# Kernel optimization log

Hardware: AMD Instinct MI355X
Metric: run time of the kernel (lower is better)

## Reference

```python
import jax, jax.numpy as jnp
import numpy as np

HEADS = 8
DIM_HEAD = 32
GROUPS = 8
EPS = 1e-5


def setup_inputs() -> dict:
    key = jax.random.key(0)
    k0, k1, k2 = jax.random.split(key, 3)
    dim = 256
    inner = HEADS * DIM_HEAD  # 256
    x = jax.random.normal(k0, (1, dim, 16, 16, 16), dtype=jnp.float32)
    gn_weight = jnp.ones((dim,), dtype=jnp.float32)
    gn_bias = jnp.zeros((dim,), dtype=jnp.float32)
    w_qkv = jax.random.normal(k1, (3 * inner, dim), dtype=jnp.float32) * 0.02
    w_out = jax.random.normal(k2, (dim, inner), dtype=jnp.float32) * 0.02
    b_out = jnp.zeros((dim,), dtype=jnp.float32)
    return {"x": x, "gn_weight": gn_weight, "gn_bias": gn_bias,
            "w_qkv": w_qkv, "w_out": w_out, "b_out": b_out}


def reference(x, gn_weight, gn_bias, w_qkv, w_out, b_out):
    b, c, d, h, w = x.shape
    n = d * h * w  # tokens

    # --- GroupNorm(8, c) with affine ---
    xg = x.reshape(b, GROUPS, c // GROUPS, n)
    mean = xg.mean(axis=(2, 3), keepdims=True)
    var = xg.var(axis=(2, 3), keepdims=True)
    xn = ((xg - mean) * jax.lax.rsqrt(var + EPS)).reshape(b, c, n)
    xn = xn * gn_weight[:, None] + gn_bias[:, None]

    # --- 1x1 Conv3d QKV projection (no bias) ---
    qkv = jnp.einsum('bcn,oc->bon', xn, w_qkv)              # (b, 3*H*dh, n)
    qkv = qkv.reshape(b, 3, HEADS, DIM_HEAD, n)
    q, k, v = qkv[:, 0], qkv[:, 1], qkv[:, 2]               # each (b, H, dh, n)

    # --- naive softmax attention over n = d*h*w tokens ---
    scale = DIM_HEAD ** (-0.5)
    sim = jnp.einsum('bhdi,bhdj->bhij', q, k) * scale       # (b, H, n, n)
    attn = jax.nn.softmax(sim, axis=-1)
    out = jnp.einsum('bhij,bhdj->bhdi', attn, v)            # (b, H, dh, n)
    out = out.reshape(b, HEADS * DIM_HEAD, n)

    # --- 1x1 Conv3d output projection (with bias) ---
    y = jnp.einsum('bcn,oc->bon', out, w_out) + b_out[:, None]
    return y.reshape(b, c, d, h, w)
```

## Files before the change

### kernel.cpp

```cpp
#include <hip/hip_runtime.h>
#include <hip/hip_bf16.h>
#include <math.h>


#define LOG2E 1.4426950408889634f

typedef __attribute__((ext_vector_type(8))) short bf16x8;
typedef __attribute__((ext_vector_type(4))) short bf16x4;
typedef __attribute__((ext_vector_type(4))) float f32x4;
typedef __attribute__((ext_vector_type(4))) unsigned short u16x4;

__device__ inline unsigned short f2bf(float f) {
  __hip_bfloat16 h = __float2bfloat16(f);
  return *reinterpret_cast<unsigned short*>(&h);
}

__device__ inline bf16x4 pack4_bf(float p0, float p1, float p2, float p3) {
  float2 a, b;
  a.x = p0; a.y = p1; b.x = p2; b.y = p3;
  __hip_bfloat162 lo = __float22bfloat162_rn(a);
  __hip_bfloat162 hi = __float22bfloat162_rn(b);
  union U { __hip_bfloat162 h2[2]; bf16x4 v; } u;
  u.h2[0] = lo; u.h2[1] = hi;
  return u.v;
}

__global__ __launch_bounds__(256) void xt_kernel(const float* __restrict__ x,
                                                 unsigned short* __restrict__ xTb) {
  __shared__ float tile[64][65];
  int nb = blockIdx.x * 64, cb = blockIdx.y * 64;
  int tn = threadIdx.x & 63, t4 = threadIdx.x >> 6;
#pragma unroll
  for (int i = 0; i < 16; ++i) {
    int cc = t4 + i * 4;
    tile[cc][tn] = x[(size_t)(cb + cc) * 4096 + nb + tn];
  }
  __syncthreads();
#pragma unroll
  for (int i = 0; i < 16; ++i) {
    int nn = t4 + i * 4;
    xTb[(size_t)(nb + nn) * 256 + cb + tn] = f2bf(tile[tn][nn]);
  }
}

__global__ __launch_bounds__(256) void gn_part_kernel(const float* __restrict__ x,
                                                      float* __restrict__ psum) {
  int bi = blockIdx.x;
  const float4* p = reinterpret_cast<const float4*>(x) + (size_t)bi * 512 + threadIdx.x;
  float4 v1 = p[0];
  float4 v2 = p[256];
  float s = (v1.x + v1.y) + (v1.z + v1.w) + (v2.x + v2.y) + (v2.z + v2.w);
  float q = (v1.x * v1.x + v1.y * v1.y) + (v1.z * v1.z + v1.w * v1.w) +
            (v2.x * v2.x + v2.y * v2.y) + (v2.z * v2.z + v2.w * v2.w);
  for (int off = 32; off > 0; off >>= 1) {
    s += __shfl_down(s, off);
    q += __shfl_down(q, off);
  }
  __shared__ float ss[4], sq[4];
  int w = threadIdx.x >> 6, lane = threadIdx.x & 63;
  if (lane == 0) { ss[w] = s; sq[w] = q; }
  __syncthreads();
  if (threadIdx.x == 0) {
    psum[bi * 2 + 0] = (ss[0] + ss[1]) + (ss[2] + ss[3]);
    psum[bi * 2 + 1] = (sq[0] + sq[1]) + (sq[2] + sq[3]);
  }
}

__global__ __launch_bounds__(64) void gn_final_kernel(const float* __restrict__ psum,
                                                      float* __restrict__ stats) {
  int g = blockIdx.x;
  int lane = threadIdx.x;
  float s = psum[(g * 64 + lane) * 2 + 0];
  float q = psum[(g * 64 + lane) * 2 + 1];
  for (int off = 32; off > 0; off >>= 1) {
    s += __shfl_down(s, off);
    q += __shfl_down(q, off);
  }
  if (lane == 0) {
    float mean = s * (1.f / 131072.f);
    float var = q * (1.f / 131072.f) - mean * mean;
    stats[g * 2 + 0] = mean;
    stats[g * 2 + 1] = rsqrtf(var + 1e-5f);
  }
}

__global__ __launch_bounds__(256) void fold_kernel(const float* __restrict__ w_qkv,
                                                   const float* __restrict__ gnw,
                                                   const float* __restrict__ gnb,
                                                   const float* __restrict__ stats,
                                                   unsigned short* __restrict__ w2b,
                                                   float* __restrict__ bias0) {
  int wid = (blockIdx.x * 256 + threadIdx.x) >> 6;
  int lane = threadIdx.x & 63;
  float part = 0.f;
#pragma unroll
  for (int cc = 0; cc < 4; ++cc) {
    int c = lane + cc * 64;
    int g = c >> 5;
    float mean = stats[2 * g], rstd = stats[2 * g + 1];
    float al = rstd * gnw[c];
    float be = gnb[c] - mean * al;
    float wv = w_qkv[wid * 256 + c];
    w2b[wid * 256 + c] = f2bf(wv * al);
    part += wv * be;
  }
  for (int off = 32; off > 0; off >>= 1) part += __shfl_down(part, off);
  if (lane == 0) bias0[wid] = part;
}

__global__ __launch_bounds__(256) void wout_cast_kernel(const float* __restrict__ w_out,
                                                        unsigned short* __restrict__ w_outb) {
  int i = (blockIdx.x * 256 + threadIdx.x) * 4;
  float4 v = *(const float4*)(w_out + i);
  u16x4 o;
  o[0] = f2bf(v.x); o[1] = f2bf(v.y); o[2] = f2bf(v.z); o[3] = f2bf(v.w);
  *(u16x4*)(w_outb + i) = o;
}

__global__ __launch_bounds__(256) void gemm_qkv_mfma(const unsigned short* __restrict__ w2b,
                                                     const unsigned short* __restrict__ xTb,
                                                     const float* __restrict__ bias0,
                                                     unsigned short* __restrict__ qt,
                                                     unsigned short* __restrict__ ktb,
                                                     unsigned short* __restrict__ v16) {
  const int nb = blockIdx.x, mb = blockIdx.y;
  const int t = threadIdx.x;
  const int w = t >> 6, lane = t & 63;
  const int c = lane & 15, g = lane >> 4;
  const int m0 = mb * 64 + w * 16;
  const int n0 = nb * 64;
  const f32x4 zero4 = {0.f, 0.f, 0.f, 0.f};

  const unsigned short* ap = w2b + (size_t)(m0 + c) * 256 + g * 8;
  bf16x8 af[8];
#pragma unroll
  for (int ks = 0; ks < 8; ++ks) af[ks] = *(const bf16x8*)(ap + ks * 32);

  f32x4 acc[4] = {zero4, zero4, zero4, zero4};
  const unsigned short* bp = xTb + (size_t)(n0 + c) * 256 + g * 8;
#pragma unroll
  for (int half = 0; half < 2; ++half) {
    bf16x8 bf[4][4];
#pragma unroll
    for (int nt = 0; nt < 4; ++nt)
#pragma unroll
      for (int k2 = 0; k2 < 4; ++k2)
        bf[nt][k2] = *(const bf16x8*)(bp + (size_t)nt * 4096 + half * 128 + k2 * 32);
#pragma unroll
    for (int k2 = 0; k2 < 4; ++k2)
#pragma unroll
      for (int nt = 0; nt < 4; ++nt)
        acc[nt] = __builtin_amdgcn_mfma_f32_16x16x32_bf16(af[half * 4 + k2], bf[nt][k2],
                                                          acc[nt], 0, 0, 0);
  }

  const int o0 = m0 + g * 4;
  const int t3 = o0 >> 8;
  const int h = (o0 >> 5) & 7;
  const int d0 = o0 & 31;
  float b4[4];
#pragma unroll
  for (int r = 0; r < 4; ++r) b4[r] = bias0[o0 + r];
#pragma unroll
  for (int nt = 0; nt < 4; ++nt) {
    int n = n0 + nt * 16 + c;
    if (t3 == 0) {
      u16x4 v;
#pragma unroll
      for (int r = 0; r < 4; ++r) v[r] = f2bf((acc[nt][r] + b4[r]) * 0.17677669529663687f);
      *(u16x4*)(qt + (size_t)(h * 4096 + n) * 32 + d0) = v;
    } else if (t3 == 1) {
      u16x4 v;
#pragma unroll
      for (int r = 0; r < 4; ++r) v[r] = f2bf(acc[nt][r] + b4[r]);
      *(u16x4*)(ktb + (size_t)(h * 4096 + n) * 32 + d0) = v;
    } else {
#pragma unroll
      for (int r = 0; r < 4; ++r)
        v16[(size_t)((h * 256 + (n >> 4)) * 32 + d0 + r) * 16 + (n & 15)] =
            f2bf(acc[nt][r] + b4[r]);
    }
  }
}

__global__ __launch_bounds__(256) void attn_mfma_kernel(const unsigned short* __restrict__ qt,
                                                        const unsigned short* __restrict__ ktb,
                                                        const unsigned short* __restrict__ v16,
                                                        unsigned short* __restrict__ outTb) {
  const int b = blockIdx.x;
  const int h = b & 7;
  const int i0 = (b >> 3) * 64;
  const int t = threadIdx.x;
  const int w = t >> 6;
  const int lane = t & 63;
  const int c = lane & 15;
  const int g = lane >> 4;
  const f32x4 zero4 = {0.f, 0.f, 0.f, 0.f};

  const unsigned short* qb = qt + (size_t)h * 131072 + (size_t)(i0 + c) * 32 + g * 8;
  bf16x8 qf[4];
#pragma unroll
  for (int it = 0; it < 4; ++it) qf[it] = *(const bf16x8*)(qb + it * 512);

  const unsigned short* kp = ktb + (size_t)h * 131072 + (size_t)(w * 1024 + c) * 32 + g * 8;
  const unsigned short* vp = v16 + (size_t)((h * 256 + w * 64) * 32 + c) * 16 + g * 4;

  float l[4] = {0.f, 0.f, 0.f, 0.f};
  f32x4 oacc[4][2];
#pragma unroll
  for (int it = 0; it < 4; ++it) {
    oacc[it][0] = zero4;
    oacc[it][1] = zero4;
  }

  bf16x8 kf[4], kn[4];
#pragma unroll
  for (int js = 0; js < 4; ++js) kf[js] = *(const bf16x8*)(kp + js * 512);

#pragma unroll 1
  for (int jt = 0; jt < 16; ++jt) {
    bf16x4 vf[2][4];
#pragma unroll
    for (int dh = 0; dh < 2; ++dh)
#pragma unroll
      for (int js = 0; js < 4; ++js)
        vf[dh][js] = *(const bf16x4*)(vp + (jt * 4 + js) * 512 + dh * 256);
    int jn = (jt < 15) ? jt + 1 : 15;
#pragma unroll
    for (int js = 0; js < 4; ++js)
      kn[js] = *(const bf16x8*)(kp + jn * 2048 + js * 512);

#pragma unroll
    for (int it = 0; it < 4; ++it) {
      f32x4 st[4];
#pragma unroll
      for (int js = 0; js < 4; ++js)
        st[js] = __builtin_amdgcn_mfma_f32_16x16x32_bf16(kf[js], qf[it], zero4, 0, 0, 0);
      bf16x4 pb[4];
      float lsum = 0.f;
#pragma unroll
      for (int js = 0; js < 4; ++js) {
        float p0 = __builtin_amdgcn_exp2f(st[js][0] * LOG2E);
        float p1 = __builtin_amdgcn_exp2f(st[js][1] * LOG2E);
        float p2 = __builtin_amdgcn_exp2f(st[js][2] * LOG2E);
        float p3 = __builtin_amdgcn_exp2f(st[js][3] * LOG2E);
        lsum += (p0 + p1) + (p2 + p3);
        pb[js] = pack4_bf(p0, p1, p2, p3);
      }
      l[it] += lsum;
#pragma unroll
      for (int js = 0; js < 4; ++js) {
        oacc[it][0] = __builtin_amdgcn_mfma_f32_16x16x16bf16_1k(vf[0][js], pb[js], oacc[it][0], 0, 0, 0);
        oacc[it][1] = __builtin_amdgcn_mfma_f32_16x16x16bf16_1k(vf[1][js], pb[js], oacc[it][1], 0, 0, 0);
      }
    }
#pragma unroll
    for (int js = 0; js < 4; ++js) kf[js] = kn[js];
  }

  __shared__ float lds_o[4][4][2][4][4][17];
  __shared__ float lds_l[4][4][16];
#pragma unroll
  for (int it = 0; it < 4; ++it) {
    float lv = l[it];
    lv += __shfl_xor(lv, 16);
    lv += __shfl_xor(lv, 32);
    if (g == 0) lds_l[w][it][c] = lv;
#pragma unroll
    for (int dh = 0; dh < 2; ++dh)
#pragma unroll
      for (int r = 0; r < 4; ++r)
        lds_o[w][it][dh][g][r][c] = oacc[it][dh][r];
  }
  __syncthreads();
  {
    const int it = w;
    float L = (lds_l[0][it][c] + lds_l[1][it][c]) + (lds_l[2][it][c] + lds_l[3][it][c]);
    float inv = 1.f / L;
#pragma unroll
    for (int dh = 0; dh < 2; ++dh) {
      u16x4 o;
#pragma unroll
      for (int r = 0; r < 4; ++r) {
        float v = ((lds_o[0][it][dh][g][r][c] + lds_o[1][it][dh][g][r][c]) +
                   (lds_o[2][it][dh][g][r][c] + lds_o[3][it][dh][g][r][c]));
        o[r] = f2bf(v * inv);
      }
      *(u16x4*)(outTb + (size_t)(i0 + it * 16 + c) * 256 + h * 32 + dh * 16 + g * 4) = o;
    }
  }
}

__global__ __launch_bounds__(256) void gemm_out_mfma(const unsigned short* __restrict__ w_outb,
                                                     const unsigned short* __restrict__ outTb,
                                                     const float* __restrict__ bias,
                                                     float* __restrict__ y) {
  const int nb = blockIdx.x, mb = blockIdx.y;
  const int t = threadIdx.x;
  const int w = t >> 6, lane = t & 63;
  const int c = lane & 15, g = lane >> 4;
  const int m0 = mb * 64 + w * 16;
  const int n0 = nb * 64;
  const f32x4 zero4 = {0.f, 0.f, 0.f, 0.f};

  const unsigned short* ap = w_outb + (size_t)(m0 + c) * 256 + g * 8;
  bf16x8 af[8];
#pragma unroll
  for (int ks = 0; ks < 8; ++ks) af[ks] = *(const bf16x8*)(ap + ks * 32);

  f32x4 acc[4] = {zero4, zero4, zero4, zero4};
  const unsigned short* bp = outTb + (size_t)(n0 + c) * 256 + g * 8;
#pragma unroll
  for (int half = 0; half < 2; ++half) {
    bf16x8 bf[4][4];
#pragma unroll
    for (int nt = 0; nt < 4; ++nt)
#pragma unroll
      for (int k2 = 0; k2 < 4; ++k2)
        bf[nt][k2] = *(const bf16x8*)(bp + (size_t)nt * 4096 + half * 128 + k2 * 32);
#pragma unroll
    for (int k2 = 0; k2 < 4; ++k2)
#pragma unroll
      for (int nt = 0; nt < 4; ++nt)
        acc[nt] = __builtin_amdgcn_mfma_f32_16x16x32_bf16(af[half * 4 + k2], bf[nt][k2],
                                                          acc[nt], 0, 0, 0);
  }

  const int o0 = m0 + g * 4;
  float b4[4];
#pragma unroll
  for (int r = 0; r < 4; ++r) b4[r] = bias[o0 + r];
#pragma unroll
  for (int nt = 0; nt < 4; ++nt) {
    int n = n0 + nt * 16 + c;
#pragma unroll
    for (int r = 0; r < 4; ++r)
      y[(size_t)(o0 + r) * 4096 + n] = acc[nt][r] + b4[r];
  }
}

extern "C" void kernel_launch(void* const* d_in, const int* in_sizes, int n_in,
                              void* d_out, int out_size, void* d_ws, size_t ws_size,
                              hipStream_t stream) {
  const float* x = (const float*)d_in[0];
  const float* gnw = (const float*)d_in[1];
  const float* gnb = (const float*)d_in[2];
  const float* w_qkv = (const float*)d_in[3];
  const float* w_out = (const float*)d_in[4];
  const float* b_out = (const float*)d_in[5];
  float* ws = (float*)d_ws;

  float* psum = ws;
  float* stats = ws + 1024;
  float* bias0 = ws + 1088;
  unsigned short* w2b = (unsigned short*)(ws + 2048);
  unsigned short* w_outb = w2b + 196608;
  unsigned short* xTb = w_outb + 65536;
  unsigned short* qt = xTb + 1048576;
  unsigned short* ktb = qt + 1048576;
  unsigned short* v16 = ktb + 1048576;
  unsigned short* outTb = v16 + 1048576;
  float* y = (float*)d_out;

  hipLaunchKernelGGL(xt_kernel, dim3(64, 4), dim3(256), 0, stream, x, xTb);
  hipLaunchKernelGGL(gn_part_kernel, dim3(512), dim3(256), 0, stream, x, psum);
  hipLaunchKernelGGL(gn_final_kernel, dim3(8), dim3(64), 0, stream, psum, stats);
  hipLaunchKernelGGL(fold_kernel, dim3(192), dim3(256), 0, stream, w_qkv, gnw, gnb, stats, w2b, bias0);
  hipLaunchKernelGGL(wout_cast_kernel, dim3(64), dim3(256), 0, stream, w_out, w_outb);
  hipLaunchKernelGGL(gemm_qkv_mfma, dim3(64, 12), dim3(256), 0, stream, w2b, xTb, bias0, qt, ktb, v16);
  hipLaunchKernelGGL(attn_mfma_kernel, dim3(512), dim3(256), 0, stream, qt, ktb, v16, outTb);
  hipLaunchKernelGGL(gemm_out_mfma, dim3(64, 4), dim3(256), 0, stream, w_outb, outTb, b_out, y);
}
```

Baseline: 74.62 us.

## Fuse GroupNorm stats into transpose, merge fold kernels, widen attention to 8 waves

Computes the GroupNorm partial sums inside the transpose kernel and merges the stats-finalize, weight-fold and w_out cast into one kernel, cutting the launch count from eight to five and avoiding a second read of x. Folds log2(e) into the Q scale so the softmax exp2 needs no multiply. The attention kernel now runs 512 threads, splitting the key range across 8 waves, and raises wave priority around the MFMA sections. The cost is a larger cross-wave LDS reduction and more register pressure per block.

```diff
diff --git a/kernel.cpp b/kernel.cpp
--- a/kernel.cpp
+++ b/kernel.cpp
@@ -2,8 +2,6 @@
 #include <hip/hip_bf16.h>
 #include <math.h>
 
-
-#define LOG2E 1.4426950408889634f
 
 typedef __attribute__((ext_vector_type(8))) short bf16x8;
 typedef __attribute__((ext_vector_type(4))) short bf16x4;
@@ -25,17 +23,39 @@
   return u.v;
 }
 
-__global__ __launch_bounds__(256) void xt_kernel(const float* __restrict__ x,
-                                                 unsigned short* __restrict__ xTb) {
+__global__ __launch_bounds__(256) void xt_gn_kernel(const float* __restrict__ x,
+                                                    unsigned short* __restrict__ xTb,
+                                                    float2* __restrict__ psum2) {
   __shared__ float tile[64][65];
+  __shared__ float red[4][4];
   int nb = blockIdx.x * 64, cb = blockIdx.y * 64;
   int tn = threadIdx.x & 63, t4 = threadIdx.x >> 6;
+  float slo = 0.f, qlo = 0.f, shi = 0.f, qhi = 0.f;
 #pragma unroll
   for (int i = 0; i < 16; ++i) {
     int cc = t4 + i * 4;
-    tile[cc][tn] = x[(size_t)(cb + cc) * 4096 + nb + tn];
+    float v = x[(size_t)(cb + cc) * 4096 + nb + tn];
+    tile[cc][tn] = v;
+    if (i < 8) { slo += v; qlo += v * v; } else { shi += v; qhi += v * v; }
+  }
+#pragma unroll
+  for (int off = 32; off > 0; off >>= 1) {
+    slo += __shfl_down(slo, off); qlo += __shfl_down(qlo, off);
+    shi += __shfl_down(shi, off); qhi += __shfl_down(qhi, off);
+  }
+  if ((threadIdx.x & 63) == 0) {
+    red[t4][0] = slo; red[t4][1] = qlo; red[t4][2] = shi; red[t4][3] = qhi;
   }
   __syncthreads();
+  if (threadIdx.x == 0) {
+    float a = (red[0][0] + red[1][0]) + (red[2][0] + red[3][0]);
+    float b = (red[0][1] + red[1][1]) + (red[2][1] + red[3][1]);
+    psum2[(blockIdx.y * 2) * 64 + blockIdx.x] = make_float2(a, b);
+  } else if (threadIdx.x == 64) {
+    float a = (red[0][2] + red[1][2]) + (red[2][2] + red[3][2]);
+    float b = (red[0][3] + red[1][3]) + (red[2][3] + red[3][3]);
+    psum2[(blockIdx.y * 2 + 1) * 64 + blockIdx.x] = make_float2(a, b);
+  }
 #pragma unroll
   for (int i = 0; i < 16; ++i) {
     int nn = t4 + i * 4;
@@ -43,78 +63,67 @@
   }
 }
 
-__global__ __launch_bounds__(256) void gn_part_kernel(const float* __restrict__ x,
-                                                      float* __restrict__ psum) {
-  int bi = blockIdx.x;
-  const float4* p = reinterpret_cast<const float4*>(x) + (size_t)bi * 512 + threadIdx.x;
-  float4 v1 = p[0];
-  float4 v2 = p[256];
-  float s = (v1.x + v1.y) + (v1.z + v1.w) + (v2.x + v2.y) + (v2.z + v2.w);
-  float q = (v1.x * v1.x + v1.y * v1.y) + (v1.z * v1.z + v1.w * v1.w) +
-            (v2.x * v2.x + v2.y * v2.y) + (v2.z * v2.z + v2.w * v2.w);
-  for (int off = 32; off > 0; off >>= 1) {
-    s += __shfl_down(s, off);
-    q += __shfl_down(q, off);
-  }
-  __shared__ float ss[4], sq[4];
-  int w = threadIdx.x >> 6, lane = threadIdx.x & 63;
-  if (lane == 0) { ss[w] = s; sq[w] = q; }
+__global__ __launch_bounds__(256) void fold_all_kernel(const float* __restrict__ w_qkv,
+                                                       const float* __restrict__ gnw,
+                                                       const float* __restrict__ gnb,
+                                                       const float2* __restrict__ psum2,
+                                                       const float* __restrict__ w_out,
+                                                       unsigned short* __restrict__ w2b,
+                                                       float* __restrict__ bias0,
+                                                       unsigned short* __restrict__ w_outb) {
+  int bid = blockIdx.x;
+  int t = threadIdx.x;
+  if (bid >= 192) {
+    int i = ((bid - 192) * 256 + t) * 4;
+    float4 v = *(const float4*)(w_out + i);
+    u16x4 o;
+    o[0] = f2bf(v.x); o[1] = f2bf(v.y); o[2] = f2bf(v.z); o[3] = f2bf(v.w);
+    *(u16x4*)(w_outb + i) = o;
+    return;
+  }
+  __shared__ float sm[8], sr[8];
+  __shared__ float s_al[256], s_be[256];
+  {
+    int g = t >> 5, ii = t & 31;
+    float2 p0 = psum2[g * 64 + ii];
+    float2 p1 = psum2[g * 64 + 32 + ii];
+    float s = p0.x + p1.x, q = p0.y + p1.y;
+#pragma unroll
+    for (int off = 16; off > 0; off >>= 1) {
+      s += __shfl_xor(s, off);
+      q += __shfl_xor(q, off);
+    }
+    if (ii == 0) {
+      float mean = s * (1.f / 131072.f);
+      float var = q * (1.f / 131072.f) - mean * mean;
+      sm[g] = mean;
+      sr[g] = rsqrtf(var + 1e-5f);
+    }
+  }
   __syncthreads();
-  if (threadIdx.x == 0) {
-    psum[bi * 2 + 0] = (ss[0] + ss[1]) + (ss[2] + ss[3]);
-    psum[bi * 2 + 1] = (sq[0] + sq[1]) + (sq[2] + sq[3]);
-  }
-}
-
-__global__ __launch_bounds__(64) void gn_final_kernel(const float* __restrict__ psum,
-                                                      float* __restrict__ stats) {
-  int g = blockIdx.x;
-  int lane = threadIdx.x;
-  float s = psum[(g * 64 + lane) * 2 + 0];
-  float q = psum[(g * 64 + lane) * 2 + 1];
-  for (int off = 32; off > 0; off >>= 1) {
-    s += __shfl_down(s, off);
-    q += __shfl_down(q, off);
-  }
-  if (lane == 0) {
-    float mean = s * (1.f / 131072.f);
-    float var = q * (1.f / 131072.f) - mean * mean;
-    stats[g * 2 + 0] = mean;
-    stats[g * 2 + 1] = rsqrtf(var + 1e-5f);
-  }
-}
-
-__global__ __launch_bounds__(256) void fold_kernel(const float* __restrict__ w_qkv,
-                                                   const float* __restrict__ gnw,
-                                                   const float* __restrict__ gnb,
-                                                   const float* __restrict__ stats,
-                                                   unsigned short* __restrict__ w2b,
-                                                   float* __restrict__ bias0) {
-  int wid = (blockIdx.x * 256 + threadIdx.x) >> 6;
-  int lane = threadIdx.x & 63;
-  float part = 0.f;
-#pragma unroll
-  for (int cc = 0; cc < 4; ++cc) {
-    int c = lane + cc * 64;
-    int g = c >> 5;
-    float mean = stats[2 * g], rstd = stats[2 * g + 1];
+  {
+    int c = t, gg = c >> 5;
+    float mean = sm[gg], rstd = sr[gg];
     float al = rstd * gnw[c];
-    float be = gnb[c] - mean * al;
-    float wv = w_qkv[wid * 256 + c];
-    w2b[wid * 256 + c] = f2bf(wv * al);
-    part += wv * be;
-  }
+    s_al[c] = al;
+    s_be[c] = gnb[c] - mean * al;
+  }
+  __syncthreads();
+  int w = t >> 6, lane = t & 63;
+  int row = bid * 4 + w;
+  float4 v = *(const float4*)(w_qkv + row * 256 + lane * 4);
+  int c0 = lane * 4;
+  float part = (v.x * s_be[c0] + v.y * s_be[c0 + 1]) +
+               (v.z * s_be[c0 + 2] + v.w * s_be[c0 + 3]);
+  u16x4 o;
+  o[0] = f2bf(v.x * s_al[c0]);
+  o[1] = f2bf(v.y * s_al[c0 + 1]);
+  o[2] = f2bf(v.z * s_al[c0 + 2]);
+  o[3] = f2bf(v.w * s_al[c0 + 3]);
+  *(u16x4*)(w2b + row * 256 + c0) = o;
+#pragma unroll
   for (int off = 32; off > 0; off >>= 1) part += __shfl_down(part, off);
-  if (lane == 0) bias0[wid] = part;
-}
-
-__global__ __launch_bounds__(256) void wout_cast_kernel(const float* __restrict__ w_out,
-                                                        unsigned short* __restrict__ w_outb) {
-  int i = (blockIdx.x * 256 + threadIdx.x) * 4;
-  float4 v = *(const float4*)(w_out + i);
-  u16x4 o;
-  o[0] = f2bf(v.x); o[1] = f2bf(v.y); o[2] = f2bf(v.z); o[3] = f2bf(v.w);
-  *(u16x4*)(w_outb + i) = o;
+  if (lane == 0) bias0[row] = part;
 }
 
 __global__ __launch_bounds__(256) void gemm_qkv_mfma(const unsigned short* __restrict__ w2b,
@@ -161,13 +170,14 @@
   float b4[4];
 #pragma unroll
   for (int r = 0; r < 4; ++r) b4[r] = bias0[o0 + r];
+  const float qs = 0.17677669529663687f * 1.4426950408889634f;
 #pragma unroll
   for (int nt = 0; nt < 4; ++nt) {
     int n = n0 + nt * 16 + c;
     if (t3 == 0) {
       u16x4 v;
 #pragma unroll
-      for (int r = 0; r < 4; ++r) v[r] = f2bf((acc[nt][r] + b4[r]) * 0.17677669529663687f);
+      for (int r = 0; r < 4; ++r) v[r] = f2bf((acc[nt][r] + b4[r]) * qs);
       *(u16x4*)(qt + (size_t)(h * 4096 + n) * 32 + d0) = v;
     } else if (t3 == 1) {
       u16x4 v;
@@ -183,7 +193,7 @@
   }
 }
 
-__global__ __launch_bounds__(256) void attn_mfma_kernel(const unsigned short* __restrict__ qt,
+__global__ __launch_bounds__(512) void attn_mfma_kernel(const unsigned short* __restrict__ qt,
                                                         const unsigned short* __restrict__ ktb,
                                                         const unsigned short* __restrict__ v16,
                                                         unsigned short* __restrict__ outTb) {
@@ -202,8 +212,8 @@
 #pragma unroll
   for (int it = 0; it < 4; ++it) qf[it] = *(const bf16x8*)(qb + it * 512);
 
-  const unsigned short* kp = ktb + (size_t)h * 131072 + (size_t)(w * 1024 + c) * 32 + g * 8;
-  const unsigned short* vp = v16 + (size_t)((h * 256 + w * 64) * 32 + c) * 16 + g * 4;
+  const unsigned short* kp = ktb + (size_t)h * 131072 + (size_t)(w * 512 + c) * 32 + g * 8;
+  const unsigned short* vp = v16 + (size_t)((h * 256 + w * 32) * 32 + c) * 16 + g * 4;
 
   float l[4] = {0.f, 0.f, 0.f, 0.f};
   f32x4 oacc[4][2];
@@ -218,14 +228,14 @@
   for (int js = 0; js < 4; ++js) kf[js] = *(const bf16x8*)(kp + js * 512);
 
 #pragma unroll 1
-  for (int jt = 0; jt < 16; ++jt) {
+  for (int jt = 0; jt < 8; ++jt) {
     bf16x4 vf[2][4];
 #pragma unroll
     for (int dh = 0; dh < 2; ++dh)
 #pragma unroll
       for (int js = 0; js < 4; ++js)
         vf[dh][js] = *(const bf16x4*)(vp + (jt * 4 + js) * 512 + dh * 256);
-    int jn = (jt < 15) ? jt + 1 : 15;
+    int jn = (jt < 7) ? jt + 1 : 7;
 #pragma unroll
     for (int js = 0; js < 4; ++js)
       kn[js] = *(const bf16x8*)(kp + jn * 2048 + js * 512);
@@ -233,33 +243,37 @@
 #pragma unroll
     for (int it = 0; it < 4; ++it) {
       f32x4 st[4];
+      __builtin_amdgcn_s_setprio(1);
 #pragma unroll
       for (int js = 0; js < 4; ++js)
         st[js] = __builtin_amdgcn_mfma_f32_16x16x32_bf16(kf[js], qf[it], zero4, 0, 0, 0);
+      __builtin_amdgcn_s_setprio(0);
       bf16x4 pb[4];
       float lsum = 0.f;
 #pragma unroll
       for (int js = 0; js < 4; ++js) {
-        float p0 = __builtin_amdgcn_exp2f(st[js][0] * LOG2E);
-        float p1 = __builtin_amdgcn_exp2f(st[js][1] * LOG2E);
-        float p2 = __builtin_amdgcn_exp2f(st[js][2] * LOG2E);
-        float p3 = __builtin_amdgcn_exp2f(st[js][3] * LOG2E);
+        float p0 = __builtin_amdgcn_exp2f(st[js][0]);
+        float p1 = __builtin_amdgcn_exp2f(st[js][1]);
+        float p2 = __builtin_amdgcn_exp2f(st[js][2]);
+        float p3 = __builtin_amdgcn_exp2f(st[js][3]);
         lsum += (p0 + p1) + (p2 + p3);
         pb[js] = pack4_bf(p0, p1, p2, p3);
       }
       l[it] += lsum;
+      __builtin_amdgcn_s_setprio(1);
 #pragma unroll
       for (int js = 0; js < 4; ++js) {
         oacc[it][0] = __builtin_amdgcn_mfma_f32_16x16x16bf16_1k(vf[0][js], pb[js], oacc[it][0], 0, 0, 0);
         oacc[it][1] = __builtin_amdgcn_mfma_f32_16x16x16bf16_1k(vf[1][js], pb[js], oacc[it][1], 0, 0, 0);
       }
+      __builtin_amdgcn_s_setprio(0);
     }
 #pragma unroll
     for (int js = 0; js < 4; ++js) kf[js] = kn[js];
   }
 
-  __shared__ float lds_o[4][4][2][4][4][17];
-  __shared__ float lds_l[4][4][16];
+  __shared__ float lds_o[8][4][2][4][4][17];
+  __shared__ float lds_l[8][4][16];
 #pragma unroll
   for (int it = 0; it < 4; ++it) {
     float lv = l[it];
@@ -274,20 +288,21 @@
   }
   __syncthreads();
   {
-    const int it = w;
-    float L = (lds_l[0][it][c] + lds_l[1][it][c]) + (lds_l[2][it][c] + lds_l[3][it][c]);
+    const int it = w & 3;
+    const int dh = w >> 2;
+    float L = ((lds_l[0][it][c] + lds_l[1][it][c]) + (lds_l[2][it][c] + lds_l[3][it][c])) +
+              ((lds_l[4][it][c] + lds_l[5][it][c]) + (lds_l[6][it][c] + lds_l[7][it][c]));
     float inv = 1.f / L;
-#pragma unroll
-    for (int dh = 0; dh < 2; ++dh) {
-      u16x4 o;
-#pragma unroll
-      for (int r = 0; r < 4; ++r) {
-        float v = ((lds_o[0][it][dh][g][r][c] + lds_o[1][it][dh][g][r][c]) +
-                   (lds_o[2][it][dh][g][r][c] + lds_o[3][it][dh][g][r][c]));
-        o[r] = f2bf(v * inv);
-      }
-      *(u16x4*)(outTb + (size_t)(i0 + it * 16 + c) * 256 + h * 32 + dh * 16 + g * 4) = o;
-    }
+    u16x4 o;
+#pragma unroll
+    for (int r = 0; r < 4; ++r) {
+      float v = ((lds_o[0][it][dh][g][r][c] + lds_o[1][it][dh][g][r][c]) +
+                 (lds_o[2][it][dh][g][r][c] + lds_o[3][it][dh][g][r][c])) +
+                ((lds_o[4][it][dh][g][r][c] + lds_o[5][it][dh][g][r][c]) +
+                 (lds_o[6][it][dh][g][r][c] + lds_o[7][it][dh][g][r][c]));
+      o[r] = f2bf(v * inv);
+    }
+    *(u16x4*)(outTb + (size_t)(i0 + it * 16 + c) * 256 + h * 32 + dh * 16 + g * 4) = o;
   }
 }
 
@@ -350,8 +365,7 @@
   const float* b_out = (const float*)d_in[5];
   float* ws = (float*)d_ws;
 
-  float* psum = ws;
-  float* stats = ws + 1024;
+  float2* psum2 = (float2*)ws;
   float* bias0 = ws + 1088;
   unsigned short* w2b = (unsigned short*)(ws + 2048);
   unsigned short* w_outb = w2b + 196608;
@@ -362,12 +376,10 @@
   unsigned short* outTb = v16 + 1048576;
   float* y = (float*)d_out;
 
-  hipLaunchKernelGGL(xt_kernel, dim3(64, 4), dim3(256), 0, stream, x, xTb);
-  hipLaunchKernelGGL(gn_part_kernel, dim3(512), dim3(256), 0, stream, x, psum);
-  hipLaunchKernelGGL(gn_final_kernel, dim3(8), dim3(64), 0, stream, psum, stats);
-  hipLaunchKernelGGL(fold_kernel, dim3(192), dim3(256), 0, stream, w_qkv, gnw, gnb, stats, w2b, bias0);
-  hipLaunchKernelGGL(wout_cast_kernel, dim3(64), dim3(256), 0, stream, w_out, w_outb);
+  hipLaunchKernelGGL(xt_gn_kernel, dim3(64, 4), dim3(256), 0, stream, x, xTb, psum2);
+  hipLaunchKernelGGL(fold_all_kernel, dim3(256), dim3(256), 0, stream, w_qkv, gnw, gnb,
+                     psum2, w_out, w2b, bias0, w_outb);
   hipLaunchKernelGGL(gemm_qkv_mfma, dim3(64, 12), dim3(256), 0, stream, w2b, xTb, bias0, qt, ktb, v16);
-  hipLaunchKernelGGL(attn_mfma_kernel, dim3(512), dim3(256), 0, stream, qt, ktb, v16, outTb);
+  hipLaunchKernelGGL(attn_mfma_kernel, dim3(512), dim3(512), 0, stream, qt, ktb, v16, outTb);
   hipLaunchKernelGGL(gemm_out_mfma, dim3(64, 4), dim3(256), 0, stream, w_outb, outTb, b_out, y);
 }
```

After: 69.78 us. -6.5%, faster.
